# Performance work log

Hardware: AMD Instinct MI355X
Metric: run time of the kernel (lower is better)

Reference implementation:

```python
import jax, jax.numpy as jnp
import numpy as np

B, S, D, FF, E, TOP_K = 4, 2048, 1024, 4096, 8, 2


def setup_inputs() -> dict:
    key = jax.random.key(0)
    ks = jax.random.split(key, 13)
    sd = 1.0 / np.sqrt(D)
    sf = 1.0 / np.sqrt(FF)
    return {
        "x":   jax.random.normal(ks[0], (B, S, D), jnp.float32),
        # parallel 2-way router
        "Wr":  jax.random.normal(ks[1], (D, 2), jnp.float32) * sd,
        "br":  jnp.zeros((2,), jnp.float32),
        # MoE gate
        "Wg":  jax.random.normal(ks[2], (D, E), jnp.float32) * sd,
        "bg":  jnp.zeros((E,), jnp.float32),
        # expert FFNs
        "W1":  jax.random.normal(ks[3], (E, D, FF), jnp.float32) * sd,
        "b1":  jnp.zeros((E, FF), jnp.float32),
        "W2":  jax.random.normal(ks[4], (E, FF, D), jnp.float32) * sf,
        "b2":  jnp.zeros((E, D), jnp.float32),
        # dense FFN
        "D1":  jax.random.normal(ks[5], (D, FF), jnp.float32) * sd,
        "d1b": jnp.zeros((FF,), jnp.float32),
        "D2":  jax.random.normal(ks[6], (FF, D), jnp.float32) * sf,
        "d2b": jnp.zeros((D,), jnp.float32),
    }


def _hybrid_moe(x, Wr, br, Wg, bg, W1, b1, W2, b2, D1, d1b, D2, d2b):
    b, s, d = x.shape
    t = x.reshape(-1, d)                                  # [T, D]
    T = t.shape[0]

    # parallel 2-way blend router
    rp = jax.nn.softmax(x @ Wr + br, axis=-1)             # [B, S, 2]

    # MoE gating: softmax over experts, top-k, renormalize
    gp = jax.nn.softmax(t @ Wg + bg, axis=-1)             # [T, E]
    vals, idx = jax.lax.top_k(gp, TOP_K)                  # [T, K]
    vals = vals / jnp.sum(vals, axis=-1, keepdims=True)
    cw = jnp.zeros((T, E), t.dtype).at[jnp.arange(T)[:, None], idx].add(vals)  # [T, E]

    # expert FFNs (ReLU MLP), combined with top-k weights
    h = jax.nn.relu(jnp.einsum('td,edf->tef', t, W1) + b1)       # [T, E, FF]
    eo = jnp.einsum('tef,efd->ted', h, W2) + b2                  # [T, E, D]
    moe = jnp.einsum('te,ted->td', cw, eo).reshape(b, s, d)

    # dense FFN branch
    dense = jax.nn.relu(x @ D1 + d1b) @ D2 + d2b

    return rp[..., 0:1] * moe + rp[..., 1:2] * dense


def reference(x, Wr, br, Wg, bg, W1, b1, W2, b2, D1, d1b, D2, d2b):
    return _hybrid_moe(x, Wr, br, Wg, bg, W1, b1, W2, b2, D1, d1b, D2, d2b)
```

## Files before the change

kernel.cpp:

```cpp
#include <hip/hip_runtime.h>
#include <stdint.h>

#define T_TOK   8192
#define D_DIM   1024
#define FF_DIM  4096
#define E_NUM   8
#define SLOT_MAX 18432
#define RT_MAX  104

typedef unsigned int   u32;
typedef unsigned short u16;
typedef __attribute__((ext_vector_type(4))) float  f32x4;
typedef __attribute__((ext_vector_type(4))) float  f4;
typedef __attribute__((ext_vector_type(8))) short  bf16x8;
typedef __attribute__((ext_vector_type(8))) unsigned short u16x8;
typedef __attribute__((ext_vector_type(4))) unsigned short u16x4;

__device__ __forceinline__ u16 f2bf(float f) {
  u32 u = __builtin_bit_cast(u32, f);
  return (u16)((u + 0x7fffu + ((u >> 16) & 1u)) >> 16);
}
__device__ __forceinline__ float bf2f(u16 h) {
  u32 u = ((u32)h) << 16; return __builtin_bit_cast(float, u);
}

typedef const __attribute__((address_space(1))) u32* gp1_t;
typedef __attribute__((address_space(3))) u32*       lp3_t;
__device__ __forceinline__ void gload16(const u16* g, u16* l) {
  __builtin_amdgcn_global_load_lds((gp1_t)(const void*)g, (lp3_t)l, 16, 0, 0);
}

__global__ __launch_bounds__(256) void k_route(
    const float* __restrict__ x, const float* __restrict__ Wr, const float* __restrict__ br,
    const float* __restrict__ Wg, const float* __restrict__ bg,
    int* __restrict__ hdr, int4* __restrict__ tok_sel, float4* __restrict__ tok_wf,
    u16* __restrict__ xb)
{
  int w = threadIdx.x >> 6, l = threadIdx.x & 63;
  int t = blockIdx.x * 4 + w;
  const float* xt = x + (size_t)t * D_DIM;
  u16* xbt = xb + (size_t)t * D_DIM;
  float p[10];
  #pragma unroll
  for (int i = 0; i < 10; ++i) p[i] = 0.f;
  #pragma unroll
  for (int j = 0; j < 4; ++j) {
    int d0 = j * 256 + l * 4;
    f4 xv = *(const f4*)&xt[d0];
    u16x4 xo; xo[0]=f2bf(xv[0]); xo[1]=f2bf(xv[1]); xo[2]=f2bf(xv[2]); xo[3]=f2bf(xv[3]);
    *(u16x4*)&xbt[d0] = xo;
    f4 wra = *(const f4*)&Wr[d0 * 2];
    f4 wrb = *(const f4*)&Wr[d0 * 2 + 4];
    p[0] += xv[0]*wra[0] + xv[1]*wra[2] + xv[2]*wrb[0] + xv[3]*wrb[2];
    p[1] += xv[0]*wra[1] + xv[1]*wra[3] + xv[2]*wrb[1] + xv[3]*wrb[3];
    #pragma unroll
    for (int i = 0; i < 4; ++i) {
      f4 g0 = *(const f4*)&Wg[(size_t)(d0 + i) * 8];
      f4 g1 = *(const f4*)&Wg[(size_t)(d0 + i) * 8 + 4];
      p[2] += xv[i]*g0[0]; p[3] += xv[i]*g0[1]; p[4] += xv[i]*g0[2]; p[5] += xv[i]*g0[3];
      p[6] += xv[i]*g1[0]; p[7] += xv[i]*g1[1]; p[8] += xv[i]*g1[2]; p[9] += xv[i]*g1[3];
    }
  }
  #pragma unroll
  for (int off = 32; off; off >>= 1) {
    #pragma unroll
    for (int i = 0; i < 10; ++i) p[i] += __shfl_xor(p[i], off, 64);
  }
  if (l == 0) {
    float a0 = p[0] + br[0], a1 = p[1] + br[1];
    float m  = fmaxf(a0, a1);
    float e0 = __expf(a0 - m), e1 = __expf(a1 - m);
    float rs = 1.f / (e0 + e1);
    float rp0 = e0 * rs, rp1 = e1 * rs;
    float g[E_NUM]; float gm = -1e30f;
    #pragma unroll
    for (int e = 0; e < E_NUM; ++e) { g[e] = p[2 + e] + bg[e]; gm = fmaxf(gm, g[e]); }
    int i0 = 0;
    #pragma unroll
    for (int e = 1; e < E_NUM; ++e) if (g[e] > g[i0]) i0 = e;
    int i1 = (i0 == 0) ? 1 : 0;
    #pragma unroll
    for (int e = 0; e < E_NUM; ++e) if (e != i0 && g[e] > g[i1]) i1 = e;
    float x0 = __expf(g[i0] - gm), x1 = __expf(g[i1] - gm);
    float s = 1.f / (x0 + x1);
    int r0 = atomicAdd(&hdr[i0], 1);
    int r1 = atomicAdd(&hdr[i1], 1);
    tok_sel[t] = make_int4(i0, r0, i1, r1);
    tok_wf[t]  = make_float4(x0 * s, x1 * s, rp0, rp1);
  }
}

__global__ __launch_bounds__(256) void k_setup(
    int* __restrict__ hdr, int4* __restrict__ tilemap, int* __restrict__ perm,
    const int4* __restrict__ tok_sel, int2* __restrict__ tok_slot)
{
  __shared__ int soff[E_NUM + 1];
  int tid = threadIdx.x;
  if (tid == 0) {
    int acc = 0;
    for (int e = 0; e < E_NUM; ++e) {
      soff[e] = acc; hdr[8 + e] = acc;
      acc += (hdr[e] + 255) & ~255;
    }
    soff[E_NUM] = acc;
    hdr[16] = acc;
    hdr[17] = acc >> 8;
    hdr[18] = (acc >> 8) + T_TOK / 256;
  }
  __syncthreads();
  int nmoe = soff[E_NUM] >> 8;
  for (int rt = tid; rt < RT_MAX; rt += 256) {
    int4 ent;
    if (rt < nmoe) {
      int row0 = rt * 256;
      int e = 0;
      while (e < E_NUM - 1 && row0 >= soff[e + 1]) ++e;
      ent = make_int4(0, row0, e, 0);
    } else if (rt < nmoe + T_TOK / 256) {
      ent = make_int4(1, (rt - nmoe) * 256, -1, 0);
    } else {
      ent = make_int4(-1, 0, 0, 0);
    }
    tilemap[rt] = ent;
  }
  for (int s = tid; s < SLOT_MAX; s += 256) perm[s] = -1;
  __syncthreads();
  for (int t = tid; t < T_TOK; t += 256) {
    int4 s = tok_sel[t];
    int s0 = soff[s.x] + s.y;
    int s1 = soff[s.z] + s.w;
    perm[s0] = t; perm[s1] = t;
    tok_slot[t] = make_int2(s0, s1);
  }
}

__global__ __launch_bounds__(256) void k_tcast_all(
    const float* __restrict__ W1, const float* __restrict__ W2,
    const float* __restrict__ D1, const float* __restrict__ D2,
    u16* __restrict__ W1bt, u16* __restrict__ W2bt,
    u16* __restrict__ D1bt, u16* __restrict__ D2bt)
{
  int bid = blockIdx.x;
  int panel = bid >> 10, pb = bid & 1023;
  const float* s; u16* d; int R, C, ltc;
  if (panel < 8)       { s = W1 + (size_t)panel * D_DIM * FF_DIM; d = W1bt + (size_t)panel * D_DIM * FF_DIM; R = D_DIM;  C = FF_DIM; ltc = 6; }
  else if (panel < 16) { int e = panel - 8;
                         s = W2 + (size_t)e * FF_DIM * D_DIM;     d = W2bt + (size_t)e * FF_DIM * D_DIM;     R = FF_DIM; C = D_DIM;  ltc = 4; }
  else if (panel == 16){ s = D1; d = D1bt; R = D_DIM;  C = FF_DIM; ltc = 6; }
  else                 { s = D2; d = D2bt; R = FF_DIM; C = D_DIM;  ltc = 4; }
  int tc = pb & ((1 << ltc) - 1), tr = pb >> ltc;

  __shared__ float tile[64][65];
  int t = threadIdx.x;
  #pragma unroll
  for (int p = 0; p < 4; ++p) {
    int r = p * 16 + (t >> 4);
    int c4 = (t & 15) * 4;
    f4 v = *(const f4*)&s[(size_t)(tr * 64 + r) * C + tc * 64 + c4];
    tile[r][c4+0] = v[0]; tile[r][c4+1] = v[1]; tile[r][c4+2] = v[2]; tile[r][c4+3] = v[3];
  }
  __syncthreads();
  #pragma unroll
  for (int q = 0; q < 2; ++q) {
    int oc = q * 32 + (t >> 3);
    int r8 = (t & 7) * 8;
    u16x8 o;
    #pragma unroll
    for (int j = 0; j < 8; ++j) o[j] = f2bf(tile[r8 + j][oc]);
    *(u16x8*)&d[(size_t)(tc * 64 + oc) * R + tr * 64 + r8] = o;
  }
}

#define LGKM0() { asm volatile("s_waitcnt lgkmcnt(0)" ::: "memory"); \
                  __builtin_amdgcn_sched_barrier(0); }
#define BAR()   __builtin_amdgcn_s_barrier()

template <int RELU, int GATHER>
__global__ __launch_bounds__(512, 2) void k_gemm8p(
    const u16* __restrict__ Amoe, const u16* __restrict__ Aden,
    const u16* __restrict__ Bexp, const u16* __restrict__ Bden,
    const float* __restrict__ biasexp, const float* __restrict__ biasden,
    u16* __restrict__ Omoe, u16* __restrict__ Oden,
    const int* __restrict__ hdr, const int4* __restrict__ tilemap,
    const int* __restrict__ perm,
    int K, int N, long bexp_stride, int biasexp_stride, int lg2gx)
{
  int gx  = 1 << lg2gx;
  int nwg = gx * gridDim.y;
  int lin = blockIdx.y * gx + blockIdx.x;
  int sw  = (lin & 7) * (nwg >> 3) + (lin >> 3);
  int ct  = sw & (gx - 1);
  int rt  = sw >> lg2gx;
  if (rt >= hdr[18]) return;

  int4 ent = tilemap[rt];
  const u16* B; const float* bias; u16* O;
  if (ent.x == 1) { B = Bden; bias = biasden; O = Oden; }
  else {
    B = Bexp + (size_t)ent.z * bexp_stride;
    bias = biasexp + (size_t)ent.z * biasexp_stride;
    O = Omoe;
  }
  const int row0 = ent.y;

  __shared__ __align__(16) u16 lds[65536];

  const int tid = threadIdx.x;
  const int wid = tid >> 6, l = tid & 63;
  const int wm = wid >> 2, wn = wid & 3;

  const int srow = wid * 8 + (l >> 3);
  const int skel = ((l & 7) ^ (l >> 3)) * 8;
  const u16* aSrcP[4];
  const u16* bSrcP[4];
  #pragma unroll
  for (int i = 0; i < 4; ++i) {
    int r = srow + i * 64;
    if (ent.x == 1)      aSrcP[i] = Aden + (size_t)(row0 + r) * K + skel;
    else if (GATHER) {
      int pr = perm[row0 + r]; pr = pr < 0 ? 0 : pr;
      aSrcP[i] = Amoe + (size_t)pr * K + skel;
    } else               aSrcP[i] = Amoe + (size_t)(row0 + r) * K + skel;
    bSrcP[i] = B + (size_t)(ct * 256 + r) * K + skel;
  }

  const int fr = l & 15, fq = l >> 4;
  const int fx = (l & 7) << 4;
  const int cs0 = (fq * 16) ^ fx;
  const int cs1 = (64 + fq * 16) ^ fx;
  const int brow = (wn & 1) * 64;
  const char* ldsc = (const char*)lds;
  const char* aP0 = ldsc + wm * 16384 + fr * 128 + cs0;
  const char* aP1 = ldsc + wm * 16384 + fr * 128 + cs1;
  const char* bP0 = ldsc + 65536 + (wn >> 1) * 16384 + (brow + fr) * 128 + cs0;
  const char* bP1 = ldsc + 65536 + (wn >> 1) * 16384 + (brow + fr) * 128 + cs1;

  auto STAGE_A = [&](int tt, int h, int bb) {
    u16* dst = &lds[(bb * 2 + h) * 8192 + wid * 512];
    gload16(aSrcP[h * 2]     + tt * 64, dst);
    gload16(aSrcP[h * 2 + 1] + tt * 64, dst + 4096);
  };
  auto STAGE_B = [&](int tt, int h, int bb) {
    u16* dst = &lds[32768 + (bb * 2 + h) * 8192 + wid * 512];
    gload16(bSrcP[h * 2]     + tt * 64, dst);
    gload16(bSrcP[h * 2 + 1] + tt * 64, dst + 4096);
  };

  f32x4 acc[8][4];
  #pragma unroll
  for (int m = 0; m < 8; ++m)
    #pragma unroll
    for (int n = 0; n < 4; ++n) acc[m][n] = (f32x4){0.f, 0.f, 0.f, 0.f};

  bf16x8 a0[4][2], a1[4][2], b0[2][2], b1[2][2];

  #define READ_A0(B_) { _Pragma("unroll") for (int j = 0; j < 4; ++j) { \
      a0[j][0] = *(const bf16x8*)(aP0 + ((B_)*32768 + j*2048)); \
      a0[j][1] = *(const bf16x8*)(aP1 + ((B_)*32768 + j*2048)); } }
  #define READ_A1(B_) { _Pragma("unroll") for (int j = 0; j < 4; ++j) { \
      a1[j][0] = *(const bf16x8*)(aP0 + ((B_)*32768 + 8192 + j*2048)); \
      a1[j][1] = *(const bf16x8*)(aP1 + ((B_)*32768 + 8192 + j*2048)); } }
  #define READ_B0(B_) { _Pragma("unroll") for (int i = 0; i < 2; ++i) { \
      b0[i][0] = *(const bf16x8*)(bP0 + ((B_)*32768 + i*2048)); \
      b0[i][1] = *(const bf16x8*)(bP1 + ((B_)*32768 + i*2048)); } }
  #define READ_B1(B_) { _Pragma("unroll") for (int i = 0; i < 2; ++i) { \
      b1[i][0] = *(const bf16x8*)(bP0 + ((B_)*32768 + 4096 + i*2048)); \
      b1[i][1] = *(const bf16x8*)(bP1 + ((B_)*32768 + 4096 + i*2048)); } }
  #define MFMA_Q(am, bm, mo, no) { __builtin_amdgcn_s_setprio(1); \
    _Pragma("unroll") for (int j = 0; j < 4; ++j) \
      _Pragma("unroll") for (int i = 0; i < 2; ++i) { \
        acc[(mo) + j][(no) + i] = __builtin_amdgcn_mfma_f32_16x16x32_bf16(am[j][0], bm[i][0], acc[(mo) + j][(no) + i], 0, 0, 0); \
        acc[(mo) + j][(no) + i] = __builtin_amdgcn_mfma_f32_16x16x32_bf16(am[j][1], bm[i][1], acc[(mo) + j][(no) + i], 0, 0, 0); } \
    __builtin_amdgcn_s_setprio(0); }

  const int NK = K >> 6;

  STAGE_B(0, 0, 0); STAGE_B(0, 1, 0); STAGE_A(0, 0, 0); STAGE_A(0, 1, 0);
  STAGE_B(1, 0, 1); STAGE_B(1, 1, 1); STAGE_A(1, 0, 1);
  asm volatile("s_waitcnt vmcnt(6)" ::: "memory");
  BAR();

  #define TILE(B_, t_) { \
     \
    READ_A0(B_); READ_B0(B_); \
    if ((t_) + 1 < NK) STAGE_A((t_) + 1, 1, (B_) ^ 1); \
    BAR(); LGKM0(); \
    MFMA_Q(a0, b0, 0, 0); \
    BAR(); \
     \
    READ_B1(B_); \
    BAR(); LGKM0(); \
    MFMA_Q(a0, b1, 0, 2); \
    BAR(); \
     \
    READ_A1(B_); \
    if ((t_) + 2 < NK) STAGE_B((t_) + 2, 0, (B_)); \
    BAR(); LGKM0(); \
    MFMA_Q(a1, b1, 4, 2); \
    BAR(); \
     \
    if ((t_) + 2 < NK) { STAGE_B((t_) + 2, 1, (B_)); STAGE_A((t_) + 2, 0, (B_)); } \
    BAR(); \
    MFMA_Q(a1, b0, 4, 0); \
    if ((t_) < NK - 2) { asm volatile("s_waitcnt vmcnt(6)" ::: "memory"); } \
    else               { asm volatile("s_waitcnt vmcnt(0)" ::: "memory"); } \
    BAR(); \
    __builtin_amdgcn_sched_barrier(0); }

  for (int t = 0; t < NK; t += 2) {
    TILE(0, t);
    TILE(1, t + 1);
  }
  #undef TILE

  __syncthreads();
  float bv[4];
  #pragma unroll
  for (int ni = 0; ni < 4; ++ni) bv[ni] = bias[ct * 256 + wn * 64 + ni * 16 + fr];
  float* ep = (float*)((char*)lds + wid * 4608);
  const int row16 = l >> 2, cg = l & 3;
  #pragma unroll
  for (int mi = 0; mi < 8; ++mi) {
    #pragma unroll
    for (int ni = 0; ni < 4; ++ni) {
      f32x4 v = acc[mi][ni];
      #pragma unroll
      for (int j = 0; j < 4; ++j) {
        float f = v[j] + bv[ni];
        if (RELU) f = fmaxf(f, 0.f);
        ep[(fq * 4 + j) * 68 + ni * 16 + fr] = f;
      }
    }
    #pragma unroll
    for (int p = 0; p < 2; ++p) {
      f4 r0 = *(f4*)&ep[row16 * 68 + (cg + p * 4) * 8];
      f4 r1 = *(f4*)&ep[row16 * 68 + (cg + p * 4) * 8 + 4];
      u16x8 o;
      o[0]=f2bf(r0[0]); o[1]=f2bf(r0[1]); o[2]=f2bf(r0[2]); o[3]=f2bf(r0[3]);
      o[4]=f2bf(r1[0]); o[5]=f2bf(r1[1]); o[6]=f2bf(r1[2]); o[7]=f2bf(r1[3]);
      int rr = row0 + wm * 128 + mi * 16 + row16;
      int cc = ct * 256 + wn * 64 + (cg + p * 4) * 8;
      *(u16x8*)&O[(size_t)rr * N + cc] = o;
    }
  }
  #undef READ_A0
  #undef READ_A1
  #undef READ_B0
  #undef READ_B1
  #undef MFMA_Q
}

__global__ __launch_bounds__(128) void k_combine(
    const u16* __restrict__ eo, const u16* __restrict__ dense_o,
    const float4* __restrict__ tok_wf, const int2* __restrict__ tok_slot,
    float* __restrict__ out)
{
  int t = blockIdx.x;
  int c8 = threadIdx.x;
  float4 wf = tok_wf[t];
  int2 sl = tok_slot[t];
  u16x8 a  = *((const u16x8*)(eo + (size_t)sl.x * D_DIM) + c8);
  u16x8 b  = *((const u16x8*)(eo + (size_t)sl.y * D_DIM) + c8);
  u16x8 dn = *((const u16x8*)(dense_o + (size_t)t * D_DIM) + c8);
  float* op = out + (size_t)t * D_DIM + c8 * 8;
  #pragma unroll
  for (int j = 0; j < 8; ++j) {
    float mo = wf.x * bf2f(a[j]) + wf.y * bf2f(b[j]);
    op[j] = wf.z * mo + wf.w * bf2f(dn[j]);
  }
}

extern "C" void kernel_launch(void* const* d_in, const int* in_sizes, int n_in,
                              void* d_out, int out_size, void* d_ws, size_t ws_size,
                              hipStream_t stream)
{
  const float* x   = (const float*)d_in[0];
  const float* Wr  = (const float*)d_in[1];
  const float* br  = (const float*)d_in[2];
  const float* Wg  = (const float*)d_in[3];
  const float* bg  = (const float*)d_in[4];
  const float* W1  = (const float*)d_in[5];
  const float* b1  = (const float*)d_in[6];
  const float* W2  = (const float*)d_in[7];
  const float* b2  = (const float*)d_in[8];
  const float* D1  = (const float*)d_in[9];
  const float* d1b = (const float*)d_in[10];
  const float* D2  = (const float*)d_in[11];
  const float* d2b = (const float*)d_in[12];
  float* out = (float*)d_out;

  char* base = (char*)d_ws;
  size_t cur = 0;
  auto alloc = [&](size_t b) -> void* {
    void* p = base + cur; cur = (cur + b + 255) & ~(size_t)255; return p;
  };
  int*    hdr      = (int*)   alloc(256 * sizeof(int));
  int4*   tilemap  = (int4*)  alloc((size_t)RT_MAX * sizeof(int4));
  int4*   tok_sel  = (int4*)  alloc((size_t)T_TOK * sizeof(int4));
  float4* tok_wf   = (float4*)alloc((size_t)T_TOK * sizeof(float4));
  int2*   tok_slot = (int2*)  alloc((size_t)T_TOK * sizeof(int2));
  int*    perm     = (int*)   alloc((size_t)SLOT_MAX * sizeof(int));
  u16*    xb       = (u16*)   alloc((size_t)T_TOK * D_DIM * 2);
  u16*    W1bt     = (u16*)   alloc((size_t)E_NUM * D_DIM * FF_DIM * 2);
  u16*    W2bt     = (u16*)   alloc((size_t)E_NUM * D_DIM * FF_DIM * 2);
  u16*    D1bt     = (u16*)   alloc((size_t)D_DIM * FF_DIM * 2);
  u16*    D2bt     = (u16*)   alloc((size_t)D_DIM * FF_DIM * 2);
  u16*    h_moe    = (u16*)   alloc((size_t)SLOT_MAX * FF_DIM * 2);
  u16*    h_dense  = (u16*)   alloc((size_t)T_TOK * FF_DIM * 2);
  u16*    eo       = (u16*)   alloc((size_t)SLOT_MAX * D_DIM * 2);
  u16*    dense_o  = (u16*)   alloc((size_t)T_TOK * D_DIM * 2);
  (void)in_sizes; (void)n_in; (void)out_size; (void)ws_size;

  hipMemsetAsync(hdr, 0, 256 * sizeof(int), stream);
  k_route    <<<T_TOK / 4, 256, 0, stream>>>(x, Wr, br, Wg, bg, hdr, tok_sel, tok_wf, xb);
  k_setup    <<<1, 256, 0, stream>>>(hdr, tilemap, perm, tok_sel, tok_slot);
  k_tcast_all<<<18 * 1024, 256, 0, stream>>>(W1, W2, D1, D2, W1bt, W2bt, D1bt, D2bt);

  k_gemm8p<1, 1><<<dim3(FF_DIM / 256, RT_MAX), 512, 0, stream>>>(
      xb, xb, W1bt, D1bt, b1, d1b, h_moe, h_dense, hdr, tilemap, perm,
      D_DIM, FF_DIM, (long)D_DIM * FF_DIM, FF_DIM, 4);
  k_gemm8p<0, 0><<<dim3(D_DIM / 256, RT_MAX), 512, 0, stream>>>(
      h_moe, h_dense, W2bt, D2bt, b2, d2b, eo, dense_o, hdr, tilemap, perm,
      FF_DIM, D_DIM, (long)D_DIM * FF_DIM, D_DIM, 2);

  k_combine<<<T_TOK, 128, 0, stream>>>(eo, dense_o, tok_wf, tok_slot, out);
}
```

Measured before the change: 780.5 us.

## Split-K the second GEMM into two halves and enlarge transpose-cast tiles

The down-projection GEMM (K=4096, N=1024) now runs split-K across two z-slices. Each slice writes a partial bf16 output to its own buffer, and the combine kernel sums the two partials. The intent is more workgroups for a GEMM that had only 4 column tiles, which should fill the CUs better. The trade-off is extra partial-output traffic and an extra bf16 rounding of each partial. Separately, the weight transpose-cast kernel now processes 128x64 tiles per block instead of 64x64, halving the block count.

```diff
diff --git a/kernel.cpp b/kernel.cpp
--- a/kernel.cpp
+++ b/kernel.cpp
@@ -141,7 +141,7 @@
     u16* __restrict__ D1bt, u16* __restrict__ D2bt)
 {
   int bid = blockIdx.x;
-  int panel = bid >> 10, pb = bid & 1023;
+  int panel = bid >> 9, pb = bid & 511;
   const float* s; u16* d; int R, C, ltc;
   if (panel < 8)       { s = W1 + (size_t)panel * D_DIM * FF_DIM; d = W1bt + (size_t)panel * D_DIM * FF_DIM; R = D_DIM;  C = FF_DIM; ltc = 6; }
   else if (panel < 16) { int e = panel - 8;
@@ -150,24 +150,24 @@
   else                 { s = D2; d = D2bt; R = FF_DIM; C = D_DIM;  ltc = 4; }
   int tc = pb & ((1 << ltc) - 1), tr = pb >> ltc;
 
-  __shared__ float tile[64][65];
+  __shared__ float tile[128][65];
   int t = threadIdx.x;
   #pragma unroll
-  for (int p = 0; p < 4; ++p) {
+  for (int p = 0; p < 8; ++p) {
     int r = p * 16 + (t >> 4);
     int c4 = (t & 15) * 4;
-    f4 v = *(const f4*)&s[(size_t)(tr * 64 + r) * C + tc * 64 + c4];
+    f4 v = *(const f4*)&s[(size_t)(tr * 128 + r) * C + tc * 64 + c4];
     tile[r][c4+0] = v[0]; tile[r][c4+1] = v[1]; tile[r][c4+2] = v[2]; tile[r][c4+3] = v[3];
   }
   __syncthreads();
   #pragma unroll
-  for (int q = 0; q < 2; ++q) {
-    int oc = q * 32 + (t >> 3);
-    int r8 = (t & 7) * 8;
+  for (int q = 0; q < 4; ++q) {
+    int oc = q * 16 + (t >> 4);
+    int r8 = (t & 15) * 8;
     u16x8 o;
     #pragma unroll
     for (int j = 0; j < 8; ++j) o[j] = f2bf(tile[r8 + j][oc]);
-    *(u16x8*)&d[(size_t)(tc * 64 + oc) * R + tr * 64 + r8] = o;
+    *(u16x8*)&d[(size_t)(tc * 64 + oc) * R + tr * 128 + r8] = o;
   }
 }
 
@@ -175,7 +175,7 @@
                   __builtin_amdgcn_sched_barrier(0); }
 #define BAR()   __builtin_amdgcn_s_barrier()
 
-template <int RELU, int GATHER>
+template <int RELU, int GATHER, int SPLITK>
 __global__ __launch_bounds__(512, 2) void k_gemm8p(
     const u16* __restrict__ Amoe, const u16* __restrict__ Aden,
     const u16* __restrict__ Bexp, const u16* __restrict__ Bden,
@@ -193,13 +193,19 @@
   int rt  = sw >> lg2gx;
   if (rt >= hdr[18]) return;
 
+  const int kz   = SPLITK ? blockIdx.z : 0;
+  const int keff = SPLITK ? (K >> 1) : K;
+  const int koff = kz * keff;
+
   int4 ent = tilemap[rt];
   const u16* B; const float* bias; u16* O;
-  if (ent.x == 1) { B = Bden; bias = biasden; O = Oden; }
-  else {
+  if (ent.x == 1) {
+    B = Bden; bias = biasden;
+    O = Oden + (size_t)kz * T_TOK * N;
+  } else {
     B = Bexp + (size_t)ent.z * bexp_stride;
     bias = biasexp + (size_t)ent.z * biasexp_stride;
-    O = Omoe;
+    O = Omoe + (size_t)kz * SLOT_MAX * N;
   }
   const int row0 = ent.y;
 
@@ -216,12 +222,12 @@
   #pragma unroll
   for (int i = 0; i < 4; ++i) {
     int r = srow + i * 64;
-    if (ent.x == 1)      aSrcP[i] = Aden + (size_t)(row0 + r) * K + skel;
+    if (ent.x == 1)      aSrcP[i] = Aden + (size_t)(row0 + r) * K + skel + koff;
     else if (GATHER) {
       int pr = perm[row0 + r]; pr = pr < 0 ? 0 : pr;
-      aSrcP[i] = Amoe + (size_t)pr * K + skel;
-    } else               aSrcP[i] = Amoe + (size_t)(row0 + r) * K + skel;
-    bSrcP[i] = B + (size_t)(ct * 256 + r) * K + skel;
+      aSrcP[i] = Amoe + (size_t)pr * K + skel + koff;
+    } else               aSrcP[i] = Amoe + (size_t)(row0 + r) * K + skel + koff;
+    bSrcP[i] = B + (size_t)(ct * 256 + r) * K + skel + koff;
   }
 
   const int fr = l & 15, fq = l >> 4;
@@ -273,7 +279,7 @@
         acc[(mo) + j][(no) + i] = __builtin_amdgcn_mfma_f32_16x16x32_bf16(am[j][1], bm[i][1], acc[(mo) + j][(no) + i], 0, 0, 0); } \
     __builtin_amdgcn_s_setprio(0); }
 
-  const int NK = K >> 6;
+  const int NK = keff >> 6;
 
   STAGE_B(0, 0, 0); STAGE_B(0, 1, 0); STAGE_A(0, 0, 0); STAGE_A(0, 1, 0);
   STAGE_B(1, 0, 1); STAGE_B(1, 1, 1); STAGE_A(1, 0, 1);
@@ -316,7 +322,8 @@
   __syncthreads();
   float bv[4];
   #pragma unroll
-  for (int ni = 0; ni < 4; ++ni) bv[ni] = bias[ct * 256 + wn * 64 + ni * 16 + fr];
+  for (int ni = 0; ni < 4; ++ni)
+    bv[ni] = (SPLITK && kz) ? 0.f : bias[ct * 256 + wn * 64 + ni * 16 + fr];
   float* ep = (float*)((char*)lds + wid * 4608);
   const int row16 = l >> 2, cg = l & 3;
   #pragma unroll
@@ -359,14 +366,22 @@
   int c8 = threadIdx.x;
   float4 wf = tok_wf[t];
   int2 sl = tok_slot[t];
+  const u16x8* eo1 = (const u16x8*)(eo + (size_t)SLOT_MAX * D_DIM);
+  const u16x8* dn1 = (const u16x8*)(dense_o + (size_t)T_TOK * D_DIM);
   u16x8 a  = *((const u16x8*)(eo + (size_t)sl.x * D_DIM) + c8);
+  u16x8 ap = *(eo1 + ((size_t)sl.x * D_DIM) / 8 + c8);
   u16x8 b  = *((const u16x8*)(eo + (size_t)sl.y * D_DIM) + c8);
+  u16x8 bp = *(eo1 + ((size_t)sl.y * D_DIM) / 8 + c8);
   u16x8 dn = *((const u16x8*)(dense_o + (size_t)t * D_DIM) + c8);
+  u16x8 dp = *(dn1 + ((size_t)t * D_DIM) / 8 + c8);
   float* op = out + (size_t)t * D_DIM + c8 * 8;
   #pragma unroll
   for (int j = 0; j < 8; ++j) {
-    float mo = wf.x * bf2f(a[j]) + wf.y * bf2f(b[j]);
-    op[j] = wf.z * mo + wf.w * bf2f(dn[j]);
+    float av = bf2f(a[j]) + bf2f(ap[j]);
+    float bvv = bf2f(b[j]) + bf2f(bp[j]);
+    float dv = bf2f(dn[j]) + bf2f(dp[j]);
+    float mo = wf.x * av + wf.y * bvv;
+    op[j] = wf.z * mo + wf.w * dv;
   }
 }
 
@@ -407,19 +422,19 @@
   u16*    D2bt     = (u16*)   alloc((size_t)D_DIM * FF_DIM * 2);
   u16*    h_moe    = (u16*)   alloc((size_t)SLOT_MAX * FF_DIM * 2);
   u16*    h_dense  = (u16*)   alloc((size_t)T_TOK * FF_DIM * 2);
-  u16*    eo       = (u16*)   alloc((size_t)SLOT_MAX * D_DIM * 2);
-  u16*    dense_o  = (u16*)   alloc((size_t)T_TOK * D_DIM * 2);
+  u16*    eo       = (u16*)   alloc((size_t)2 * SLOT_MAX * D_DIM * 2);
+  u16*    dense_o  = (u16*)   alloc((size_t)2 * T_TOK * D_DIM * 2);
   (void)in_sizes; (void)n_in; (void)out_size; (void)ws_size;
 
   hipMemsetAsync(hdr, 0, 256 * sizeof(int), stream);
   k_route    <<<T_TOK / 4, 256, 0, stream>>>(x, Wr, br, Wg, bg, hdr, tok_sel, tok_wf, xb);
   k_setup    <<<1, 256, 0, stream>>>(hdr, tilemap, perm, tok_sel, tok_slot);
-  k_tcast_all<<<18 * 1024, 256, 0, stream>>>(W1, W2, D1, D2, W1bt, W2bt, D1bt, D2bt);
-
-  k_gemm8p<1, 1><<<dim3(FF_DIM / 256, RT_MAX), 512, 0, stream>>>(
+  k_tcast_all<<<18 * 512, 256, 0, stream>>>(W1, W2, D1, D2, W1bt, W2bt, D1bt, D2bt);
+
+  k_gemm8p<1, 1, 0><<<dim3(FF_DIM / 256, RT_MAX), 512, 0, stream>>>(
       xb, xb, W1bt, D1bt, b1, d1b, h_moe, h_dense, hdr, tilemap, perm,
       D_DIM, FF_DIM, (long)D_DIM * FF_DIM, FF_DIM, 4);
-  k_gemm8p<0, 0><<<dim3(D_DIM / 256, RT_MAX), 512, 0, stream>>>(
+  k_gemm8p<0, 0, 1><<<dim3(D_DIM / 256, RT_MAX, 2), 512, 0, stream>>>(
       h_moe, h_dense, W2bt, D2bt, b2, d2b, eo, dense_o, hdr, tilemap, perm,
       FF_DIM, D_DIM, (long)D_DIM * FF_DIM, D_DIM, 2);
 
```

Result: slower. 800.3 us (+2.5%).

## Software-pipeline LDS fragment reads across MFMA phases and enlarge transpose-cast tiles

Applied to the files above, without the earlier changes.

The GEMM main loop is restructured so the LDS fragment reads for the next MFMA quarter are issued before the current quarter's MFMAs. Partial lgkmcnt and vmcnt waits replace full drains, and the tile loop is unrolled in pairs with a specialized last iteration. Separately, the weight transpose/cast kernel now handles 128x64 tiles per block with half as many blocks, giving more work per block. The finer-grained waits are meant to hide LDS latency behind MFMA issue, but they carry correctness risk if any count is off.

```diff
diff --git a/kernel.cpp b/kernel.cpp
--- a/kernel.cpp
+++ b/kernel.cpp
@@ -141,7 +141,7 @@
     u16* __restrict__ D1bt, u16* __restrict__ D2bt)
 {
   int bid = blockIdx.x;
-  int panel = bid >> 10, pb = bid & 1023;
+  int panel = bid >> 9, pb = bid & 511;
   const float* s; u16* d; int R, C, ltc;
   if (panel < 8)       { s = W1 + (size_t)panel * D_DIM * FF_DIM; d = W1bt + (size_t)panel * D_DIM * FF_DIM; R = D_DIM;  C = FF_DIM; ltc = 6; }
   else if (panel < 16) { int e = panel - 8;
@@ -150,29 +150,31 @@
   else                 { s = D2; d = D2bt; R = FF_DIM; C = D_DIM;  ltc = 4; }
   int tc = pb & ((1 << ltc) - 1), tr = pb >> ltc;
 
-  __shared__ float tile[64][65];
+  __shared__ float tile[128][65];
   int t = threadIdx.x;
   #pragma unroll
-  for (int p = 0; p < 4; ++p) {
+  for (int p = 0; p < 8; ++p) {
     int r = p * 16 + (t >> 4);
     int c4 = (t & 15) * 4;
-    f4 v = *(const f4*)&s[(size_t)(tr * 64 + r) * C + tc * 64 + c4];
+    f4 v = *(const f4*)&s[(size_t)(tr * 128 + r) * C + tc * 64 + c4];
     tile[r][c4+0] = v[0]; tile[r][c4+1] = v[1]; tile[r][c4+2] = v[2]; tile[r][c4+3] = v[3];
   }
   __syncthreads();
   #pragma unroll
-  for (int q = 0; q < 2; ++q) {
-    int oc = q * 32 + (t >> 3);
-    int r8 = (t & 7) * 8;
+  for (int q = 0; q < 4; ++q) {
+    int oc = q * 16 + (t >> 4);
+    int r8 = (t & 15) * 8;
     u16x8 o;
     #pragma unroll
     for (int j = 0; j < 8; ++j) o[j] = f2bf(tile[r8 + j][oc]);
-    *(u16x8*)&d[(size_t)(tc * 64 + oc) * R + tr * 64 + r8] = o;
-  }
-}
-
-#define LGKM0() { asm volatile("s_waitcnt lgkmcnt(0)" ::: "memory"); \
+    *(u16x8*)&d[(size_t)(tc * 64 + oc) * R + tr * 128 + r8] = o;
+  }
+}
+
+#define VMW(n)  asm volatile("s_waitcnt vmcnt(" #n ")" ::: "memory")
+#define LGKM(n) { asm volatile("s_waitcnt lgkmcnt(" #n ")" ::: "memory"); \
                   __builtin_amdgcn_sched_barrier(0); }
+#define SB()    __builtin_amdgcn_sched_barrier(0)
 #define BAR()   __builtin_amdgcn_s_barrier()
 
 template <int RELU, int GATHER>
@@ -277,41 +279,53 @@
 
   STAGE_B(0, 0, 0); STAGE_B(0, 1, 0); STAGE_A(0, 0, 0); STAGE_A(0, 1, 0);
   STAGE_B(1, 0, 1); STAGE_B(1, 1, 1); STAGE_A(1, 0, 1);
-  asm volatile("s_waitcnt vmcnt(6)" ::: "memory");
+  VMW(6);
   BAR();
-
-  #define TILE(B_, t_) { \
-     \
-    READ_A0(B_); READ_B0(B_); \
-    if ((t_) + 1 < NK) STAGE_A((t_) + 1, 1, (B_) ^ 1); \
-    BAR(); LGKM0(); \
-    MFMA_Q(a0, b0, 0, 0); \
-    BAR(); \
-     \
-    READ_B1(B_); \
-    BAR(); LGKM0(); \
-    MFMA_Q(a0, b1, 0, 2); \
-    BAR(); \
-     \
-    READ_A1(B_); \
-    if ((t_) + 2 < NK) STAGE_B((t_) + 2, 0, (B_)); \
-    BAR(); LGKM0(); \
-    MFMA_Q(a1, b1, 4, 2); \
-    BAR(); \
-     \
-    if ((t_) + 2 < NK) { STAGE_B((t_) + 2, 1, (B_)); STAGE_A((t_) + 2, 0, (B_)); } \
-    BAR(); \
-    MFMA_Q(a1, b0, 4, 0); \
-    if ((t_) < NK - 2) { asm volatile("s_waitcnt vmcnt(6)" ::: "memory"); } \
-    else               { asm volatile("s_waitcnt vmcnt(0)" ::: "memory"); } \
-    BAR(); \
-    __builtin_amdgcn_sched_barrier(0); }
-
-  for (int t = 0; t < NK; t += 2) {
-    TILE(0, t);
-    TILE(1, t + 1);
-  }
-  #undef TILE
+  READ_A0(0); READ_B0(0);
+  SB();
+
+  #define PAIR(t_, LAST_) { \
+     \
+    READ_B1(0); \
+    STAGE_A((t_) + 1, 1, 1); \
+    SB(); BAR(); LGKM(4); \
+    MFMA_Q(a0, b0, 0, 0); BAR(); \
+     \
+    VMW(8); READ_A1(0); SB(); BAR(); LGKM(8); \
+    MFMA_Q(a0, b1, 0, 2); BAR(); \
+     \
+    VMW(2); READ_A0(1); \
+    if (!(LAST_)) STAGE_B((t_) + 2, 0, 0); \
+    SB(); BAR(); LGKM(8); \
+    MFMA_Q(a1, b1, 4, 2); BAR(); \
+     \
+    READ_B1(1); \
+    if (!(LAST_)) { STAGE_B((t_) + 2, 1, 0); STAGE_A((t_) + 2, 0, 0); } \
+    SB(); BAR(); \
+    MFMA_Q(a1, b0, 4, 0); BAR(); \
+     \
+    READ_B0(1); \
+    if (!(LAST_)) STAGE_A((t_) + 2, 1, 0); \
+    SB(); BAR(); LGKM(4); \
+    MFMA_Q(a0, b1, 0, 2); BAR(); \
+     \
+    if (LAST_) { VMW(0); } else { VMW(8); } \
+    READ_A1(1); SB(); BAR(); LGKM(8); \
+    MFMA_Q(a0, b0, 0, 0); BAR(); \
+     \
+    if (!(LAST_)) { VMW(2); READ_A0(0); STAGE_B((t_) + 3, 0, 1); } \
+    SB(); BAR(); \
+    if (LAST_) { LGKM(0); } else { LGKM(8); } \
+    MFMA_Q(a1, b0, 4, 0); BAR(); \
+     \
+    if (!(LAST_)) { READ_B0(0); STAGE_B((t_) + 3, 1, 1); STAGE_A((t_) + 3, 0, 1); } \
+    SB(); BAR(); \
+    MFMA_Q(a1, b1, 4, 2); BAR(); \
+  }
+
+  for (int t = 0; t + 2 < NK; t += 2) PAIR(t, 0);
+  PAIR(NK - 2, 1);
+  #undef PAIR
 
   __syncthreads();
   float bv[4];
@@ -414,7 +428,7 @@
   hipMemsetAsync(hdr, 0, 256 * sizeof(int), stream);
   k_route    <<<T_TOK / 4, 256, 0, stream>>>(x, Wr, br, Wg, bg, hdr, tok_sel, tok_wf, xb);
   k_setup    <<<1, 256, 0, stream>>>(hdr, tilemap, perm, tok_sel, tok_slot);
-  k_tcast_all<<<18 * 1024, 256, 0, stream>>>(W1, W2, D1, D2, W1bt, W2bt, D1bt, D2bt);
+  k_tcast_all<<<18 * 512, 256, 0, stream>>>(W1, W2, D1, D2, W1bt, W2bt, D1bt, D2bt);
 
   k_gemm8p<1, 1><<<dim3(FF_DIM / 256, RT_MAX), 512, 0, stream>>>(
       xb, xb, W1bt, D1bt, b1, d1b, h_moe, h_dense, hdr, tilemap, perm,
```

Result: slower. 1.840 ms (+135.7%).
